# Kernel tuning notes

Measured on AMD Instinct MI355X. Metric: run time of the kernel, lower is better.

The kernel has to match this reference:

```python
import jax, jax.numpy as jnp
import numpy as np

B, S, C, H = 1024, 254, 2, 1024
TIME_DIM = 64
HALF = TIME_DIM // 2
N_STEPS = 50


def time_embed(t):
    # t: [B] -> [B, 64] sinusoidal embedding, matching SinusoidalEmbedding(64)
    freqs = jnp.exp(jnp.arange(HALF, dtype=jnp.float32) * (-np.log(10000.0) / (HALF - 1)))
    ang = t[:, None] * freqs[None, :]  # [B, 32]
    return jnp.concatenate([jnp.sin(ang), jnp.cos(ang)], axis=-1)  # [B, 64]


def setup_inputs() -> dict:
    key = jax.random.key(0)
    ks = jax.random.split(key, 12)
    inp = {}
    inp["state"] = jax.random.normal(ks[0], (B, S), jnp.float32)
    inp["x0"] = jax.random.normal(ks[1], (B, C), jnp.float32)  # initial noise of sample()
    dims = [S + C + TIME_DIM, H, H, H, H, C]  # 320 -> 1024 x4 -> 2
    for i in range(5):
        kw, kb = jax.random.split(ks[2 + i])
        inp[f"W{i}"] = jax.random.normal(kw, (dims[i], dims[i + 1]), jnp.float32) * (1.0 / np.sqrt(dims[i]))
        inp[f"b{i}"] = jax.random.normal(kb, (dims[i + 1],), jnp.float32) * 0.01
    return inp


def reference(state, x0, W0, b0, W1, b1, W2, b2, W3, b3, W4, b4):
    dt = 1.0 / N_STEPS

    def velocity(x, t):
        temb = time_embed(t)
        h = jnp.concatenate([state, x, temb], axis=-1)  # [B, 320]
        h = jax.nn.silu(h @ W0 + b0)
        h = jax.nn.silu(h @ W1 + b1)
        h = jax.nn.silu(h @ W2 + b2)
        h = jax.nn.silu(h @ W3 + b3)
        return h @ W4 + b4  # [B, C]

    def step(x, i):
        t = jnp.full((state.shape[0],), i * dt, dtype=jnp.float32)
        return x + dt * velocity(x, t), None

    x, _ = jax.lax.scan(step, x0, jnp.arange(N_STEPS, dtype=jnp.float32))
    return x
```

## Files before the change

kernel.cpp:

```cpp
#include <hip/hip_runtime.h>


typedef __bf16 bf16x8 __attribute__((ext_vector_type(8)));
typedef float  f32x4  __attribute__((ext_vector_type(4)));
typedef unsigned short u16;
typedef u16 u16x8 __attribute__((ext_vector_type(8)));
typedef u16 u16x4 __attribute__((ext_vector_type(4)));

#define H 1024
#define BATCH 1024
#define SDIM 254
#define NSTEP 50
#define DT 0.02f
#define LDP 40

__device__ __forceinline__ u16 f2bf(float f) {
  unsigned int u = __float_as_uint(f);
  return (u16)((u + 0x7FFFu + ((u >> 16) & 1u)) >> 16);
}

__device__ __forceinline__ float silu(float v) {
  return v / (1.0f + __expf(-v));
}

__global__ void transpose_w(const float* __restrict__ A, const float* __restrict__ B,
                            const float* __restrict__ C, u16* __restrict__ TA,
                            u16* __restrict__ TB, u16* __restrict__ TC) {
  const float* W = (blockIdx.z == 0) ? A : (blockIdx.z == 1) ? B : C;
  u16* T = (blockIdx.z == 0) ? TA : (blockIdx.z == 1) ? TB : TC;
  __shared__ float tile[32][33];
  const int n0 = blockIdx.x * 32, k0 = blockIdx.y * 32;
  const int tx = threadIdx.x & 31, ty = threadIdx.x >> 5;
#pragma unroll
  for (int i = 0; i < 4; ++i)
    tile[ty + 8 * i][tx] = W[(k0 + ty + 8 * i) * H + n0 + tx];
  __syncthreads();
#pragma unroll
  for (int i = 0; i < 4; ++i)
    T[(size_t)(n0 + ty + 8 * i) * H + k0 + tx] = f2bf(tile[tx][ty + 8 * i]);
}

__global__ void base_gemm(const float* __restrict__ state, const float* __restrict__ W0,
                          const float* __restrict__ b0, float* __restrict__ base) {
  __shared__ float srow[SDIM];
  const int b = blockIdx.x, tid = threadIdx.x;
  if (tid < SDIM) srow[tid] = state[b * SDIM + tid];
  __syncthreads();
  const int n = tid * 4;
  float4 bv = *(const float4*)&b0[n];
  float a0 = bv.x, a1 = bv.y, a2 = bv.z, a3 = bv.w;
  for (int k = 0; k < SDIM; ++k) {
    float s = srow[k];
    float4 w = *(const float4*)&W0[k * H + n];
    a0 += s * w.x; a1 += s * w.y; a2 += s * w.z; a3 += s * w.w;
  }
  float4 r = {a0, a1, a2, a3};
  *(float4*)&base[(size_t)b * H + n] = r;
}

__global__ void tvec_kernel(const float* __restrict__ W0, float* __restrict__ tvec) {
  const int s = blockIdx.x;
  const int h = blockIdx.y * 256 + threadIdx.x;
  const float t = (float)s * DT;
  float acc = 0.0f;
#pragma unroll
  for (int j = 0; j < 32; ++j) {
    float fr = __expf((float)j * (-9.210340371976184f / 31.0f));
    float ang = t * fr;
    acc += __sinf(ang) * W0[(256 + j) * H + h] + __cosf(ang) * W0[(288 + j) * H + h];
  }
  tvec[s * H + h] = acc;
}

__global__ void init_kernel(const float* __restrict__ base, const float* __restrict__ tvec,
                            const float* __restrict__ x0, const float* __restrict__ W0,
                            u16* __restrict__ h0, float* __restrict__ xout) {
  const int b = blockIdx.x, tid = threadIdx.x;
  const float xa = x0[2 * b], xb = x0[2 * b + 1];
  if (tid == 0) { xout[2 * b] = xa; xout[2 * b + 1] = xb; }
  const int n = tid * 4;
  float4 bs = *(const float4*)&base[(size_t)b * H + n];
  float4 tv = *(const float4*)&tvec[n];
  float4 wa = *(const float4*)&W0[254 * H + n];
  float4 wb = *(const float4*)&W0[255 * H + n];
  u16x4 r;
  r[0] = f2bf(silu(bs.x + tv.x + xa * wa.x + xb * wb.x));
  r[1] = f2bf(silu(bs.y + tv.y + xa * wa.y + xb * wb.y));
  r[2] = f2bf(silu(bs.z + tv.z + xa * wa.z + xb * wb.z));
  r[3] = f2bf(silu(bs.w + tv.w + xa * wa.w + xb * wb.w));
  *(u16x4*)&h0[(size_t)b * H + n] = r;
}

__global__ __launch_bounds__(64) void gemm_mfma(const u16* __restrict__ A,
                                                const u16* __restrict__ BT,
                                                const float* __restrict__ bias,
                                                void* __restrict__ out, int out_bf16) {
  __shared__ u16 As[32 * LDP];
  __shared__ u16 Bs[32 * LDP];
  const int tid = threadIdx.x;
  const int bn = blockIdx.x, bm = blockIdx.y;
  const int lr = tid & 15, quad = tid >> 4;

  const int srow = tid >> 2;
  const int skc = (tid & 3) * 8;

  const u16* Ap = A + (size_t)(bm * 32 + srow) * H + skc;
  const u16* Bp = BT + (size_t)(bn * 32 + srow) * H + skc;

  f32x4 acc[2][2] = {};

  u16x8 ga0 = *(const u16x8*)(Ap);
  u16x8 ga1 = *(const u16x8*)(Ap + 16 * H);
  u16x8 gb0 = *(const u16x8*)(Bp);
  u16x8 gb1 = *(const u16x8*)(Bp + 16 * H);

  for (int kt = 0; kt < 32; ++kt) {
    *(u16x8*)&As[srow * LDP + skc] = ga0;
    *(u16x8*)&As[(srow + 16) * LDP + skc] = ga1;
    *(u16x8*)&Bs[srow * LDP + skc] = gb0;
    *(u16x8*)&Bs[(srow + 16) * LDP + skc] = gb1;
    if (kt < 31) {
      const int off = (kt + 1) * 32;
      ga0 = *(const u16x8*)(Ap + off);
      ga1 = *(const u16x8*)(Ap + 16 * H + off);
      gb0 = *(const u16x8*)(Bp + off);
      gb1 = *(const u16x8*)(Bp + 16 * H + off);
    }
    bf16x8 a0 = *(const bf16x8*)&As[lr * LDP + quad * 8];
    bf16x8 a1 = *(const bf16x8*)&As[(16 + lr) * LDP + quad * 8];
    bf16x8 b0 = *(const bf16x8*)&Bs[lr * LDP + quad * 8];
    bf16x8 b1 = *(const bf16x8*)&Bs[(16 + lr) * LDP + quad * 8];
    acc[0][0] = __builtin_amdgcn_mfma_f32_16x16x32_bf16(a0, b0, acc[0][0], 0, 0, 0);
    acc[0][1] = __builtin_amdgcn_mfma_f32_16x16x32_bf16(a0, b1, acc[0][1], 0, 0, 0);
    acc[1][0] = __builtin_amdgcn_mfma_f32_16x16x32_bf16(a1, b0, acc[1][0], 0, 0, 0);
    acc[1][1] = __builtin_amdgcn_mfma_f32_16x16x32_bf16(a1, b1, acc[1][1], 0, 0, 0);
  }

#pragma unroll
  for (int mt = 0; mt < 2; ++mt)
#pragma unroll
    for (int nt = 0; nt < 2; ++nt) {
      const int gm = bm * 32 + mt * 16 + quad * 4;
      const int gn = bn * 32 + nt * 16 + lr;
      const float bv = bias[gn];
      f32x4 v = acc[mt][nt];
#pragma unroll
      for (int r = 0; r < 4; ++r) {
        float x = silu(v[r] + bv);
        if (out_bf16) ((u16*)out)[(size_t)(gm + r) * H + gn] = f2bf(x);
        else          ((float*)out)[(size_t)(gm + r) * H + gn] = x;
      }
    }
}

__global__ void tail_kernel(const float* __restrict__ h3, const float* __restrict__ W4,
                            const float* __restrict__ b4, float* __restrict__ x,
                            const float* __restrict__ base, const float* __restrict__ tvec,
                            const float* __restrict__ W0, u16* __restrict__ h0, int s) {
  const int b = blockIdx.x, tid = threadIdx.x;
  float s0 = 0.0f, s1 = 0.0f;
  for (int h = tid; h < H; h += 256) {
    float v = h3[(size_t)b * H + h];
    s0 += v * W4[2 * h];
    s1 += v * W4[2 * h + 1];
  }
#pragma unroll
  for (int o = 32; o > 0; o >>= 1) {
    s0 += __shfl_down(s0, o);
    s1 += __shfl_down(s1, o);
  }
  __shared__ float red[8];
  __shared__ float xs[2];
  const int w = tid >> 6;
  if ((tid & 63) == 0) { red[w * 2] = s0; red[w * 2 + 1] = s1; }
  __syncthreads();
  if (tid == 0) {
    float v0 = red[0] + red[2] + red[4] + red[6] + b4[0];
    float v1 = red[1] + red[3] + red[5] + red[7] + b4[1];
    float xa = x[2 * b] + DT * v0;
    float xb = x[2 * b + 1] + DT * v1;
    x[2 * b] = xa; x[2 * b + 1] = xb;
    xs[0] = xa; xs[1] = xb;
  }
  __syncthreads();
  if (s < NSTEP - 1) {
    const float xa = xs[0], xb = xs[1];
    const int n = tid * 4;
    float4 bs = *(const float4*)&base[(size_t)b * H + n];
    float4 tv = *(const float4*)&tvec[(size_t)(s + 1) * H + n];
    float4 wa = *(const float4*)&W0[254 * H + n];
    float4 wb = *(const float4*)&W0[255 * H + n];
    u16x4 r;
    r[0] = f2bf(silu(bs.x + tv.x + xa * wa.x + xb * wb.x));
    r[1] = f2bf(silu(bs.y + tv.y + xa * wa.y + xb * wb.y));
    r[2] = f2bf(silu(bs.z + tv.z + xa * wa.z + xb * wb.z));
    r[3] = f2bf(silu(bs.w + tv.w + xa * wa.w + xb * wb.w));
    *(u16x4*)&h0[(size_t)b * H + n] = r;
  }
}

extern "C" void kernel_launch(void* const* d_in, const int* in_sizes, int n_in,
                              void* d_out, int out_size, void* d_ws, size_t ws_size,
                              hipStream_t stream) {
  const float* state = (const float*)d_in[0];
  const float* x0    = (const float*)d_in[1];
  const float* W0    = (const float*)d_in[2];
  const float* b0    = (const float*)d_in[3];
  const float* W1    = (const float*)d_in[4];
  const float* b1    = (const float*)d_in[5];
  const float* W2    = (const float*)d_in[6];
  const float* b2    = (const float*)d_in[7];
  const float* W3    = (const float*)d_in[8];
  const float* b3    = (const float*)d_in[9];
  const float* W4    = (const float*)d_in[10];
  const float* b4    = (const float*)d_in[11];
  float* xout = (float*)d_out;

  char* ws = (char*)d_ws;
  const size_t MB = 1024 * 1024;
  float* base = (float*)(ws + 0);
  float* h3f  = (float*)(ws + 4 * MB);
  float* tvec = (float*)(ws + 8 * MB);
  u16* w1t = (u16*)(ws + 8 * MB + 256 * 1024);
  u16* w2t = (u16*)(ws + 10 * MB + 256 * 1024);
  u16* w3t = (u16*)(ws + 12 * MB + 256 * 1024);
  u16* hA  = (u16*)(ws + 14 * MB + 256 * 1024);
  u16* hB  = (u16*)(ws + 16 * MB + 256 * 1024);
  u16* hC  = (u16*)(ws + 18 * MB + 256 * 1024);

  transpose_w<<<dim3(32, 32, 3), 256, 0, stream>>>(W1, W2, W3, w1t, w2t, w3t);
  base_gemm<<<BATCH, 256, 0, stream>>>(state, W0, b0, base);
  tvec_kernel<<<dim3(NSTEP, 4), 256, 0, stream>>>(W0, tvec);
  init_kernel<<<BATCH, 256, 0, stream>>>(base, tvec, x0, W0, hA, xout);

  for (int s = 0; s < NSTEP; ++s) {
    gemm_mfma<<<dim3(32, 32), 64, 0, stream>>>(hA, w1t, b1, hB, 1);
    gemm_mfma<<<dim3(32, 32), 64, 0, stream>>>(hB, w2t, b2, hC, 1);
    gemm_mfma<<<dim3(32, 32), 64, 0, stream>>>(hC, w3t, b3, h3f, 0);
    tail_kernel<<<BATCH, 256, 0, stream>>>(h3f, W4, b4, xout, base, tvec, W0, hA, s);
  }
}
```

Measured before the change: 1.840 ms.

## Use 64x64 split-K MFMA tiles with register prefetch and LDS reduction; batch base_gemm rows

The layer GEMM moves from 32x32 tiles on one wave to 64x64 tiles on four waves. Each wave handles a quarter of K, loads fragments straight from global memory into registers with a three-stage prefetch ring, and the partial sums are reduced through LDS before bias and SiLU. This raises the MFMA work per loaded byte and removes the LDS staging of the operands, at the cost of more registers and a shared-memory reduction. base_gemm now processes 8 batch rows per block so each W0 load is reused across those rows.

```diff
diff --git a/kernel.cpp b/kernel.cpp
--- a/kernel.cpp
+++ b/kernel.cpp
@@ -12,7 +12,6 @@
 #define SDIM 254
 #define NSTEP 50
 #define DT 0.02f
-#define LDP 40
 
 __device__ __forceinline__ u16 f2bf(float f) {
   unsigned int u = __float_as_uint(f);
@@ -42,20 +41,27 @@
 
 __global__ void base_gemm(const float* __restrict__ state, const float* __restrict__ W0,
                           const float* __restrict__ b0, float* __restrict__ base) {
-  __shared__ float srow[SDIM];
-  const int b = blockIdx.x, tid = threadIdx.x;
-  if (tid < SDIM) srow[tid] = state[b * SDIM + tid];
-  __syncthreads();
-  const int n = tid * 4;
+  __shared__ float srow[8][SDIM];
+  const int bx = blockIdx.x, by = blockIdx.y, tid = threadIdx.x;
+  for (int i = tid; i < 8 * SDIM; i += 128)
+    srow[i / SDIM][i % SDIM] = state[(size_t)(by * 8 + i / SDIM) * SDIM + i % SDIM];
+  __syncthreads();
+  const int n = bx * 512 + tid * 4;
   float4 bv = *(const float4*)&b0[n];
-  float a0 = bv.x, a1 = bv.y, a2 = bv.z, a3 = bv.w;
+  f32x4 a[8];
+#pragma unroll
+  for (int r = 0; r < 8; ++r) { a[r][0] = bv.x; a[r][1] = bv.y; a[r][2] = bv.z; a[r][3] = bv.w; }
   for (int k = 0; k < SDIM; ++k) {
-    float s = srow[k];
-    float4 w = *(const float4*)&W0[k * H + n];
-    a0 += s * w.x; a1 += s * w.y; a2 += s * w.z; a3 += s * w.w;
-  }
-  float4 r = {a0, a1, a2, a3};
-  *(float4*)&base[(size_t)b * H + n] = r;
+    float4 wv = *(const float4*)&W0[(size_t)k * H + n];
+#pragma unroll
+    for (int r = 0; r < 8; ++r) {
+      float s = srow[r][k];
+      a[r][0] += s * wv.x; a[r][1] += s * wv.y; a[r][2] += s * wv.z; a[r][3] += s * wv.w;
+    }
+  }
+#pragma unroll
+  for (int r = 0; r < 8; ++r)
+    *(f32x4*)&base[(size_t)(by * 8 + r) * H + n] = a[r];
 }
 
 __global__ void tvec_kernel(const float* __restrict__ W0, float* __restrict__ tvec) {
@@ -91,66 +97,85 @@
   *(u16x4*)&h0[(size_t)b * H + n] = r;
 }
 
-__global__ __launch_bounds__(64) void gemm_mfma(const u16* __restrict__ A,
-                                                const u16* __restrict__ BT,
-                                                const float* __restrict__ bias,
-                                                void* __restrict__ out, int out_bf16) {
-  __shared__ u16 As[32 * LDP];
-  __shared__ u16 Bs[32 * LDP];
+__global__ __launch_bounds__(256) void gemm_mfma(const u16* __restrict__ A,
+                                                 const u16* __restrict__ BT,
+                                                 const float* __restrict__ bias,
+                                                 void* __restrict__ out, int out_bf16) {
+  __shared__ float red[4][32][68];
   const int tid = threadIdx.x;
+  const int w = tid >> 6, lane = tid & 63;
+  const int lr = lane & 15, quad = lane >> 4;
   const int bn = blockIdx.x, bm = blockIdx.y;
-  const int lr = tid & 15, quad = tid >> 4;
-
-  const int srow = tid >> 2;
-  const int skc = (tid & 3) * 8;
-
-  const u16* Ap = A + (size_t)(bm * 32 + srow) * H + skc;
-  const u16* Bp = BT + (size_t)(bn * 32 + srow) * H + skc;
-
-  f32x4 acc[2][2] = {};
-
-  u16x8 ga0 = *(const u16x8*)(Ap);
-  u16x8 ga1 = *(const u16x8*)(Ap + 16 * H);
-  u16x8 gb0 = *(const u16x8*)(Bp);
-  u16x8 gb1 = *(const u16x8*)(Bp + 16 * H);
-
-  for (int kt = 0; kt < 32; ++kt) {
-    *(u16x8*)&As[srow * LDP + skc] = ga0;
-    *(u16x8*)&As[(srow + 16) * LDP + skc] = ga1;
-    *(u16x8*)&Bs[srow * LDP + skc] = gb0;
-    *(u16x8*)&Bs[(srow + 16) * LDP + skc] = gb1;
-    if (kt < 31) {
-      const int off = (kt + 1) * 32;
-      ga0 = *(const u16x8*)(Ap + off);
-      ga1 = *(const u16x8*)(Ap + 16 * H + off);
-      gb0 = *(const u16x8*)(Bp + off);
-      gb1 = *(const u16x8*)(Bp + 16 * H + off);
+
+  const u16* Ap = A + (size_t)(bm * 64 + lr) * H + w * 256 + quad * 8;
+  const u16* Bp = BT + (size_t)(bn * 64 + lr) * H + w * 256 + quad * 8;
+
+  f32x4 acc[4][4] = {};
+  bf16x8 fa[3][4], fb[3][4];
+
+#define LOADSET(s, koff)                                          \
+  {                                                               \
+    _Pragma("unroll") for (int q = 0; q < 4; ++q) {               \
+      fa[s][q] = *(const bf16x8*)(Ap + q * 16 * H + (koff));      \
+      fb[s][q] = *(const bf16x8*)(Bp + q * 16 * H + (koff));      \
+    }                                                             \
+  }
+
+  LOADSET(0, 0)
+  LOADSET(1, 32)
+#pragma unroll
+  for (int it = 0; it < 8; ++it) {
+    const int cur = it % 3;
+    if (it < 6) {
+      const int nx = (it + 2) % 3;
+      LOADSET(nx, (it + 2) * 32)
     }
-    bf16x8 a0 = *(const bf16x8*)&As[lr * LDP + quad * 8];
-    bf16x8 a1 = *(const bf16x8*)&As[(16 + lr) * LDP + quad * 8];
-    bf16x8 b0 = *(const bf16x8*)&Bs[lr * LDP + quad * 8];
-    bf16x8 b1 = *(const bf16x8*)&Bs[(16 + lr) * LDP + quad * 8];
-    acc[0][0] = __builtin_amdgcn_mfma_f32_16x16x32_bf16(a0, b0, acc[0][0], 0, 0, 0);
-    acc[0][1] = __builtin_amdgcn_mfma_f32_16x16x32_bf16(a0, b1, acc[0][1], 0, 0, 0);
-    acc[1][0] = __builtin_amdgcn_mfma_f32_16x16x32_bf16(a1, b0, acc[1][0], 0, 0, 0);
-    acc[1][1] = __builtin_amdgcn_mfma_f32_16x16x32_bf16(a1, b1, acc[1][1], 0, 0, 0);
-  }
-
-#pragma unroll
-  for (int mt = 0; mt < 2; ++mt)
-#pragma unroll
-    for (int nt = 0; nt < 2; ++nt) {
-      const int gm = bm * 32 + mt * 16 + quad * 4;
-      const int gn = bn * 32 + nt * 16 + lr;
-      const float bv = bias[gn];
-      f32x4 v = acc[mt][nt];
-#pragma unroll
-      for (int r = 0; r < 4; ++r) {
-        float x = silu(v[r] + bv);
-        if (out_bf16) ((u16*)out)[(size_t)(gm + r) * H + gn] = f2bf(x);
-        else          ((float*)out)[(size_t)(gm + r) * H + gn] = x;
+#pragma unroll
+    for (int mt = 0; mt < 4; ++mt)
+#pragma unroll
+      for (int nt = 0; nt < 4; ++nt)
+        acc[mt][nt] = __builtin_amdgcn_mfma_f32_16x16x32_bf16(fa[cur][mt], fb[cur][nt],
+                                                              acc[mt][nt], 0, 0, 0);
+  }
+#undef LOADSET
+
+  const int m = tid >> 3;
+  const int n0 = (tid & 7) * 8;
+#pragma unroll
+  for (int half = 0; half < 2; ++half) {
+    if (half) __syncthreads();
+#pragma unroll
+    for (int mt = 0; mt < 2; ++mt)
+#pragma unroll
+      for (int nt = 0; nt < 4; ++nt)
+#pragma unroll
+        for (int r = 0; r < 4; ++r)
+          red[w][mt * 16 + quad * 4 + r][nt * 16 + lr] = acc[half * 2 + mt][nt][r];
+    __syncthreads();
+    const int gm = bm * 64 + half * 32 + m;
+#pragma unroll
+    for (int j = 0; j < 2; ++j) {
+      const int n = n0 + j * 4;
+      f32x4 s0 = *(const f32x4*)&red[0][m][n];
+      f32x4 s1 = *(const f32x4*)&red[1][m][n];
+      f32x4 s2 = *(const f32x4*)&red[2][m][n];
+      f32x4 s3 = *(const f32x4*)&red[3][m][n];
+      f32x4 bv = *(const f32x4*)&bias[bn * 64 + n];
+      if (out_bf16) {
+        u16x4 o;
+#pragma unroll
+        for (int r = 0; r < 4; ++r)
+          o[r] = f2bf(silu(s0[r] + s1[r] + s2[r] + s3[r] + bv[r]));
+        *(u16x4*)&((u16*)out)[(size_t)gm * H + bn * 64 + n] = o;
+      } else {
+        f32x4 o;
+#pragma unroll
+        for (int r = 0; r < 4; ++r)
+          o[r] = silu(s0[r] + s1[r] + s2[r] + s3[r] + bv[r]);
+        *(f32x4*)&((float*)out)[(size_t)gm * H + bn * 64 + n] = o;
       }
     }
+  }
 }
 
 __global__ void tail_kernel(const float* __restrict__ h3, const float* __restrict__ W4,
@@ -229,14 +254,14 @@
   u16* hC  = (u16*)(ws + 18 * MB + 256 * 1024);
 
   transpose_w<<<dim3(32, 32, 3), 256, 0, stream>>>(W1, W2, W3, w1t, w2t, w3t);
-  base_gemm<<<BATCH, 256, 0, stream>>>(state, W0, b0, base);
+  base_gemm<<<dim3(2, 128), 128, 0, stream>>>(state, W0, b0, base);
   tvec_kernel<<<dim3(NSTEP, 4), 256, 0, stream>>>(W0, tvec);
   init_kernel<<<BATCH, 256, 0, stream>>>(base, tvec, x0, W0, hA, xout);
 
   for (int s = 0; s < NSTEP; ++s) {
-    gemm_mfma<<<dim3(32, 32), 64, 0, stream>>>(hA, w1t, b1, hB, 1);
-    gemm_mfma<<<dim3(32, 32), 64, 0, stream>>>(hB, w2t, b2, hC, 1);
-    gemm_mfma<<<dim3(32, 32), 64, 0, stream>>>(hC, w3t, b3, h3f, 0);
+    gemm_mfma<<<dim3(16, 16), 256, 0, stream>>>(hA, w1t, b1, hB, 1);
+    gemm_mfma<<<dim3(16, 16), 256, 0, stream>>>(hB, w2t, b2, hC, 1);
+    gemm_mfma<<<dim3(16, 16), 256, 0, stream>>>(hC, w3t, b3, h3f, 0);
     tail_kernel<<<BATCH, 256, 0, stream>>>(h3f, W4, b4, xout, base, tvec, W0, hA, s);
   }
 }
```

New measurement: 2.123 ms. 15.3% more time.
